# Optimization experiments

Measured on AMD Instinct MI355X. Metric: run time of the kernel, lower is better.

Reference implementation:

```python
import jax, jax.numpy as jnp
import numpy as np

BN_EPS = 1e-5
LRELU_SLOPE = 0.2


def setup_inputs() -> dict:
    key = jax.random.key(0)
    ks = jax.random.split(key, 8)
    B, N, D = 32, 2048, 64      # batch, nodes per graph, latent_dim
    E = 1_000_000               # num edges
    H = 128                     # edge_hidden_dim
    Din = 2 * D + 4             # concat(z_src, z_dst, edge_attr)
    z = jax.random.normal(ks[0], (B, N, D), dtype=jnp.float32)
    edge_index = jax.random.randint(ks[1], (2, E), 0, B * N, dtype=jnp.int64)
    edge_attr = jax.random.normal(ks[2], (E, 4), dtype=jnp.float32)
    W1 = jax.random.normal(ks[3], (Din, H), dtype=jnp.float32) * (1.0 / np.sqrt(Din))
    b1 = jnp.zeros((H,), dtype=jnp.float32)
    gamma = jnp.ones((H,), dtype=jnp.float32)
    beta = jnp.zeros((H,), dtype=jnp.float32)
    W2 = jax.random.normal(ks[4], (H, 1), dtype=jnp.float32) * (1.0 / np.sqrt(H))
    b2 = jnp.zeros((1,), dtype=jnp.float32)
    return {"z": z, "edge_attr": edge_attr, "W1": W1, "b1": b1,
            "gamma": gamma, "beta": beta, "W2": W2, "b2": b2,
            "edge_index": edge_index}


def reference(z, edge_attr, W1, b1, gamma, beta, W2, b2, edge_index):
    B, N, D = z.shape
    zf = z.reshape(-1, D)                       # [B*N, D]
    src, dst = edge_index[0], edge_index[1]
    edge_batch = jnp.clip(src // N, 0, B - 1)
    edge_offsets = edge_batch * N               # batch_offsets[edge_batch]
    src_idx = src % N + edge_offsets
    dst_idx = dst % N + edge_offsets
    edge_input = jnp.concatenate([zf[src_idx], zf[dst_idx], edge_attr], axis=1)  # [E, 2D+4]
    h = edge_input @ W1 + b1                    # [E, H]
    # BatchNorm1d (training mode: biased batch stats over edge dim)
    mu = jnp.mean(h, axis=0)
    var = jnp.mean(jnp.square(h - mu), axis=0)
    h = (h - mu) * jax.lax.rsqrt(var + BN_EPS) * gamma + beta
    h = jnp.where(h >= 0, h, LRELU_SLOPE * h)   # LeakyReLU(0.2)
    return h @ W2 + b2                          # [E, 1]
```

## Files before the change

### kernel.cpp

```cpp
#include <hip/hip_runtime.h>

#define E_EDGES   1000000
#define NNODES    2048
#define HCH       128
#define KP        136
#define TILE      64
#define NTILES    (E_EDGES / TILE)
#define NSPREAD   8
#define GRID_GEMM 1024
#define ZVEC      (32 * 2048 * 64 / 4)
#define ZBLK      2048
#define WBLK      66

typedef short  shortx8 __attribute__((ext_vector_type(8)));
typedef float  floatx4 __attribute__((ext_vector_type(4)));

__device__ __forceinline__ unsigned short f2bf(float f) {
  union { float f; unsigned int u; } v; v.f = f;
  unsigned int r = (v.u + 0x7fffu + ((v.u >> 16) & 1u)) >> 16;
  return (unsigned short)r;
}
__device__ __forceinline__ void cfence() { asm volatile("" ::: "memory"); }
__device__ __forceinline__ void bar_lds() {
  asm volatile("s_waitcnt lgkmcnt(0)" ::: "memory");
  __builtin_amdgcn_s_barrier();
  cfence();
}

__global__ void k_prep(const float* __restrict__ z, const float* __restrict__ W1,
                       const float* __restrict__ b1,
                       unsigned short* __restrict__ zb, unsigned short* __restrict__ w1t,
                       float* __restrict__ gstats) {
  int bid = blockIdx.x;
  if (bid < ZBLK) {
    const float4* z4 = (const float4*)z;
    ushort4* zb4 = (ushort4*)zb;
    for (int i = bid * 256 + threadIdx.x; i < ZVEC; i += ZBLK * 256) {
      float4 v = z4[i];
      ushort4 o;
      o.x = f2bf(v.x); o.y = f2bf(v.y); o.z = f2bf(v.z); o.w = f2bf(v.w);
      zb4[i] = o;
    }
  } else if (bid < ZBLK + WBLK) {
    int idx = (bid - ZBLK) * 256 + threadIdx.x;
    int k = idx >> 7, n = idx & 127;
    w1t[n * KP + k] = f2bf(W1[idx]);
  } else {
    int tid = threadIdx.x;
    if (tid < 512) {
      int n = tid >> 2, kp = 132 + (tid & 3);
      w1t[n * KP + kp] = (kp == 132) ? f2bf(b1[n]) : (unsigned short)0;
    }
    for (int i = tid; i < NSPREAD * 2 * HCH; i += 256) gstats[i] = 0.f;
  }
}

template<bool OUT>
__global__ __launch_bounds__(256, 4)
void k_gemm(const unsigned short* __restrict__ zb,
            const unsigned short* __restrict__ w1t,
            const int* __restrict__ ei,
            const float* __restrict__ attr,
            float* __restrict__ gstats,
            const float* __restrict__ gamma,
            const float* __restrict__ beta,
            const float* __restrict__ W2,
            const float* __restrict__ b2,
            float* __restrict__ out) {
  __shared__ __align__(16) unsigned short A[2][TILE * KP];
  __shared__ float po[2][4][TILE];

  const int tid  = threadIdx.x;
  const int lane = tid & 63;
  const int w    = tid >> 6;
  const int l15  = lane & 15;
  const int quad = lane >> 4;
  const int ea   = w * 8 + (lane >> 3);
  const int eb   = ea + 32;
  const int ch   = lane & 7;

  shortx8 bfr[2][4], bfr4[2];
#pragma unroll
  for (int nt = 0; nt < 2; ++nt) {
    const unsigned short* bp = w1t + (w * 32 + nt * 16 + l15) * KP;
#pragma unroll
    for (int kk = 0; kk < 4; ++kk)
      bfr[nt][kk] = *(const shortx8*)(bp + kk * 32 + quad * 8);
    bfr4[nt] = (quad == 0) ? *(const shortx8*)(bp + 128)
                           : (shortx8){0, 0, 0, 0, 0, 0, 0, 0};
  }

  float eaf[2], ebb[2], ew2[2], b2v = 0.f;
  float ssum[2] = {0.f, 0.f}, ssq[2] = {0.f, 0.f};
  if (OUT) {
#pragma unroll
    for (int nt = 0; nt < 2; ++nt) {
      int c = w * 32 + nt * 16 + l15;
      float S = 0.f, Q = 0.f;
#pragma unroll
      for (int i = 0; i < NSPREAD; ++i) {
        S += gstats[i * 2 * HCH + c];
        Q += gstats[i * 2 * HCH + HCH + c];
      }
      float mu   = S * (1.0f / (float)E_EDGES);
      float var  = Q * (1.0f / (float)E_EDGES) - mu * mu;
      float rstd = rsqrtf(var + 1e-5f);
      float a = gamma[c] * rstd;
      eaf[nt] = a;
      ebb[nt] = beta[c] - mu * a;
      ew2[nt] = W2[c];
    }
    b2v = b2[0];
  }

  if (tid < 128) {
    int b = tid >> 6, r = tid & 63;
    ushort4 bl; bl.x = 0x3F80; bl.y = 0; bl.z = 0; bl.w = 0;
    *(ushort4*)(&A[b][0] + r * KP + 132) = bl;
  }

  auto rows_of = [&](int s_a, int d_a, int s_b, int d_b,
                     unsigned& r0, unsigned& r1, unsigned& r2, unsigned& r3) {
    r0 = (unsigned)s_a;
    r1 = (unsigned)s_b;
    r2 = ((unsigned)s_a & ~(unsigned)(NNODES - 1)) | ((unsigned)d_a & (NNODES - 1));
    r3 = ((unsigned)s_b & ~(unsigned)(NNODES - 1)) | ((unsigned)d_b & (NNODES - 1));
  };

  const int t0 = blockIdx.x;
  uint4 g0, g1, g2, g3;
  float4 av;
  int sa, da, sb, db;
  {
    int s0a = ei[t0 * TILE + ea], d0a = ei[E_EDGES + t0 * TILE + ea];
    int s0b = ei[t0 * TILE + eb], d0b = ei[E_EDGES + t0 * TILE + eb];
    if (w == 0) av = ((const float4*)attr)[t0 * TILE + tid];
    unsigned r0, r1, r2, r3;
    rows_of(s0a, d0a, s0b, d0b, r0, r1, r2, r3);
    g0 = *(const uint4*)(zb + (size_t)r0 * 64 + ch * 8);
    g1 = *(const uint4*)(zb + (size_t)r1 * 64 + ch * 8);
    g2 = *(const uint4*)(zb + (size_t)r2 * 64 + ch * 8);
    g3 = *(const uint4*)(zb + (size_t)r3 * 64 + ch * 8);
    *(uint4*)(&A[0][0] + ea * KP + ch * 8)      = g0;
    *(uint4*)(&A[0][0] + eb * KP + ch * 8)      = g1;
    *(uint4*)(&A[0][0] + ea * KP + 64 + ch * 8) = g2;
    *(uint4*)(&A[0][0] + eb * KP + 64 + ch * 8) = g3;
    if (w == 0) {
      ushort4 a0; a0.x = f2bf(av.x); a0.y = f2bf(av.y);
      a0.z = f2bf(av.z); a0.w = f2bf(av.w);
      *(ushort4*)(&A[0][0] + tid * KP + 128) = a0;
    }
    int t1 = t0 + GRID_GEMM;
    int s1a = ei[t1 * TILE + ea], d1a = ei[E_EDGES + t1 * TILE + ea];
    int s1b = ei[t1 * TILE + eb], d1b = ei[E_EDGES + t1 * TILE + eb];
    rows_of(s1a, d1a, s1b, d1b, r0, r1, r2, r3);
    g0 = *(const uint4*)(zb + (size_t)r0 * 64 + ch * 8);
    g1 = *(const uint4*)(zb + (size_t)r1 * 64 + ch * 8);
    g2 = *(const uint4*)(zb + (size_t)r2 * 64 + ch * 8);
    g3 = *(const uint4*)(zb + (size_t)r3 * 64 + ch * 8);
    if (w == 0) av = ((const float4*)attr)[t1 * TILE + tid];
    int t2 = t0 + 2 * GRID_GEMM;
    sa = ei[t2 * TILE + ea]; da = ei[E_EDGES + t2 * TILE + ea];
    sb = ei[t2 * TILE + eb]; db = ei[E_EDGES + t2 * TILE + eb];
  }
  bar_lds();

  int pp = 0, sl = 0;
  for (int tile = t0; ; ) {
    const bool more = (tile + GRID_GEMM) < NTILES;

    if (more) {
      *(uint4*)(&A[pp ^ 1][0] + ea * KP + ch * 8)      = g0;
      *(uint4*)(&A[pp ^ 1][0] + eb * KP + ch * 8)      = g1;
      *(uint4*)(&A[pp ^ 1][0] + ea * KP + 64 + ch * 8) = g2;
      *(uint4*)(&A[pp ^ 1][0] + eb * KP + 64 + ch * 8) = g3;
      if (w == 0) {
        ushort4 a0; a0.x = f2bf(av.x); a0.y = f2bf(av.y);
        a0.z = f2bf(av.z); a0.w = f2bf(av.w);
        *(ushort4*)(&A[pp ^ 1][0] + tid * KP + 128) = a0;
      }
      unsigned r0, r1, r2, r3;
      rows_of(sa, da, sb, db, r0, r1, r2, r3);
      g0 = *(const uint4*)(zb + (size_t)r0 * 64 + ch * 8);
      g1 = *(const uint4*)(zb + (size_t)r1 * 64 + ch * 8);
      g2 = *(const uint4*)(zb + (size_t)r2 * 64 + ch * 8);
      g3 = *(const uint4*)(zb + (size_t)r3 * 64 + ch * 8);
      int tn2 = tile + 2 * GRID_GEMM; if (tn2 > NTILES - 1) tn2 = NTILES - 1;
      if (w == 0) av = ((const float4*)attr)[tn2 * TILE + tid];
      int tn3 = tile + 3 * GRID_GEMM; if (tn3 > NTILES - 1) tn3 = NTILES - 1;
      sa = ei[tn3 * TILE + ea]; da = ei[E_EDGES + tn3 * TILE + ea];
      sb = ei[tn3 * TILE + eb]; db = ei[E_EDGES + tn3 * TILE + eb];
    }

    const unsigned short* Ar = &A[pp][0];
#pragma unroll
    for (int mt = 0; mt < 4; ++mt) {
      const unsigned short* ap = Ar + (mt * 16 + l15) * KP;
      shortx8 afr[4], a4;
#pragma unroll
      for (int kk = 0; kk < 4; ++kk)
        afr[kk] = *(const shortx8*)(ap + kk * 32 + quad * 8);
      a4 = (quad == 0) ? *(const shortx8*)(ap + 128)
                       : (shortx8){0, 0, 0, 0, 0, 0, 0, 0};

      floatx4 acc[2];
      acc[0] = (floatx4){0.f, 0.f, 0.f, 0.f};
      acc[1] = (floatx4){0.f, 0.f, 0.f, 0.f};
#pragma unroll
      for (int kk = 0; kk < 4; ++kk)
#pragma unroll
        for (int nt = 0; nt < 2; ++nt)
          acc[nt] = __builtin_amdgcn_mfma_f32_16x16x32_bf16(
              afr[kk], bfr[nt][kk], acc[nt], 0, 0, 0);
#pragma unroll
      for (int nt = 0; nt < 2; ++nt)
        acc[nt] = __builtin_amdgcn_mfma_f32_16x16x32_bf16(
            a4, bfr4[nt], acc[nt], 0, 0, 0);

      if (!OUT) {
#pragma unroll
        for (int nt = 0; nt < 2; ++nt) {
          float s = 0.f, qq = 0.f;
#pragma unroll
          for (int r = 0; r < 4; ++r) {
            float h = acc[nt][r];
            s += h; qq += h * h;
          }
          ssum[nt] += s; ssq[nt] += qq;
        }
      } else {
#pragma unroll
        for (int r = 0; r < 4; ++r) {
          float t = 0.f;
#pragma unroll
          for (int nt = 0; nt < 2; ++nt) {
            float h = acc[nt][r];
            float p = fmaf(eaf[nt], h, ebb[nt]);
            p = (p >= 0.f) ? p : 0.2f * p;
            t = fmaf(ew2[nt], p, t);
          }
          t += __shfl_xor(t, 1);
          t += __shfl_xor(t, 2);
          t += __shfl_xor(t, 4);
          t += __shfl_xor(t, 8);
          if (l15 == 0)
            po[sl][w][mt * 16 + quad * 4 + r] = t;
        }
      }
    }

    if (more || OUT) bar_lds();

    if (OUT && tid < TILE)
      out[tile * TILE + tid] = po[sl][0][tid] + po[sl][1][tid] +
                               po[sl][2][tid] + po[sl][3][tid] + b2v;

    if (!more) break;
    pp ^= 1; sl ^= 1;
    tile += GRID_GEMM;
  }

  if (!OUT) {
    float* gs = gstats + (blockIdx.x & (NSPREAD - 1)) * 2 * HCH;
#pragma unroll
    for (int nt = 0; nt < 2; ++nt) {
      float s = ssum[nt], qq = ssq[nt];
      s += __shfl_xor(s, 16); s += __shfl_xor(s, 32);
      qq += __shfl_xor(qq, 16); qq += __shfl_xor(qq, 32);
      if (quad == 0) {
        int c = w * 32 + nt * 16 + l15;
        atomicAdd(&gs[c], s);
        atomicAdd(&gs[HCH + c], qq);
      }
    }
  }
}

extern "C" void kernel_launch(void* const* d_in, const int* in_sizes, int n_in,
                              void* d_out, int out_size, void* d_ws, size_t ws_size,
                              hipStream_t stream) {
  const float* z     = (const float*)d_in[0];
  const float* attr  = (const float*)d_in[1];
  const float* W1    = (const float*)d_in[2];
  const float* b1    = (const float*)d_in[3];
  const float* gamma = (const float*)d_in[4];
  const float* beta  = (const float*)d_in[5];
  const float* W2    = (const float*)d_in[6];
  const float* b2    = (const float*)d_in[7];
  const int*   ei    = (const int*)d_in[8];
  float* out = (float*)d_out;

  char* ws = (char*)d_ws;
  unsigned short* zb  = (unsigned short*)ws;
  unsigned short* w1t = (unsigned short*)(ws + 8388608);
  float* gstats       = (float*)(ws + 8423424);

  k_prep<<<ZBLK + WBLK + 1, 256, 0, stream>>>(z, W1, b1, zb, w1t, gstats);
  k_gemm<false><<<GRID_GEMM, 256, 0, stream>>>(zb, w1t, ei, attr, gstats,
                                               gamma, beta, W2, b2, nullptr);
  k_gemm<true><<<GRID_GEMM, 256, 0, stream>>>(zb, w1t, ei, attr, gstats,
                                              gamma, beta, W2, b2, out);
}
```

Measured before the change: 210.5 us.

## Bin edges by source graph group so each XCD gathers from an L2-resident z slice

Adds a count/scan/scatter pre-pass that sorts edges into 8 bins by source-node range. It packs each edge into a 16-byte record: both row indices, the bf16 edge attributes and the original edge id. The GEMM blocks are mapped to bins via blockIdx&7, so each group of co-scheduled blocks gathers from roughly a 1 MB slice of the bf16 z table. The aim is to turn random gathers into mostly L2 hits. The cost is three extra small kernels, an extra read and write of all edges, and scattered output writes through the stashed edge ids.

```diff
diff --git a/kernel.cpp b/kernel.cpp
--- a/kernel.cpp
+++ b/kernel.cpp
@@ -8,9 +8,12 @@
 #define NTILES    (E_EDGES / TILE)
 #define NSPREAD   8
 #define GRID_GEMM 1024
+#define BPB       128
 #define ZVEC      (32 * 2048 * 64 / 4)
 #define ZBLK      2048
 #define WBLK      66
+#define NBIN      8
+#define CBLK      512
 
 typedef short  shortx8 __attribute__((ext_vector_type(8)));
 typedef float  floatx4 __attribute__((ext_vector_type(4)));
@@ -26,11 +29,16 @@
   __builtin_amdgcn_s_barrier();
   cfence();
 }
+__device__ __forceinline__ unsigned pack_rows(int s, int d) {
+  unsigned rs = (unsigned)s & 0xFFFFu;
+  unsigned rd = (unsigned)(((s & ~(NNODES - 1)) | (d & (NNODES - 1)))) & 0xFFFFu;
+  return rs | (rd << 16);
+}
 
 __global__ void k_prep(const float* __restrict__ z, const float* __restrict__ W1,
-                       const float* __restrict__ b1,
+                       const float* __restrict__ b1, const int* __restrict__ ei,
                        unsigned short* __restrict__ zb, unsigned short* __restrict__ w1t,
-                       float* __restrict__ gstats) {
+                       float* __restrict__ gstats, int* __restrict__ cnt) {
   int bid = blockIdx.x;
   if (bid < ZBLK) {
     const float4* z4 = (const float4*)z;
@@ -45,13 +53,71 @@
     int idx = (bid - ZBLK) * 256 + threadIdx.x;
     int k = idx >> 7, n = idx & 127;
     w1t[n * KP + k] = f2bf(W1[idx]);
-  } else {
+  } else if (bid == ZBLK + WBLK) {
     int tid = threadIdx.x;
     if (tid < 512) {
       int n = tid >> 2, kp = 132 + (tid & 3);
       w1t[n * KP + kp] = (kp == 132) ? f2bf(b1[n]) : (unsigned short)0;
     }
     for (int i = tid; i < NSPREAD * 2 * HCH; i += 256) gstats[i] = 0.f;
+  } else {
+    __shared__ int lh[NBIN];
+    int tid = threadIdx.x;
+    int cb = bid - (ZBLK + WBLK + 1);
+    if (tid < NBIN) lh[tid] = 0;
+    __syncthreads();
+    for (int e = cb * 256 + tid; e < E_EDGES; e += CBLK * 256)
+      atomicAdd(&lh[((unsigned)ei[e]) >> 13], 1);
+    __syncthreads();
+    if (tid < NBIN) cnt[cb * NBIN + tid] = lh[tid];
+  }
+}
+
+__global__ void k_scan(const int* __restrict__ cnt, int* __restrict__ base,
+                       int* __restrict__ binTile) {
+  __shared__ int tot[NBIN], S[NBIN + 1];
+  int b = threadIdx.x;
+  if (b < NBIN) {
+    int t = 0;
+    for (int blk = 0; blk < CBLK; ++blk) t += cnt[blk * NBIN + b];
+    tot[b] = t;
+  }
+  __syncthreads();
+  if (b == 0) {
+    int a = 0;
+    for (int i = 0; i < NBIN; ++i) { S[i] = a; a += tot[i]; }
+    S[NBIN] = a;
+    binTile[0] = 0;
+    for (int i = 1; i <= NBIN; ++i) binTile[i] = (S[i] + 63) >> 6;
+  }
+  __syncthreads();
+  if (b < NBIN) {
+    int run = S[b];
+    for (int blk = 0; blk < CBLK; ++blk) {
+      base[blk * NBIN + b] = run;
+      run += cnt[blk * NBIN + b];
+    }
+  }
+}
+
+__global__ __launch_bounds__(256)
+void k_scatter(const int* __restrict__ ei, const float* __restrict__ attr,
+               const int* __restrict__ base, uint4* __restrict__ recs) {
+  __shared__ int lcnt[NBIN];
+  int tid = threadIdx.x, bid = blockIdx.x;
+  if (tid < NBIN) lcnt[tid] = base[bid * NBIN + tid];
+  __syncthreads();
+  for (int e = bid * 256 + tid; e < E_EDGES; e += CBLK * 256) {
+    int s = ei[e], d = ei[E_EDGES + e];
+    float4 a = ((const float4*)attr)[e];
+    int b = ((unsigned)s) >> 13;
+    int slot = atomicAdd(&lcnt[b], 1);
+    uint4 r;
+    r.x = pack_rows(s, d);
+    r.y = (unsigned)f2bf(a.x) | ((unsigned)f2bf(a.y) << 16);
+    r.z = (unsigned)f2bf(a.z) | ((unsigned)f2bf(a.w) << 16);
+    r.w = (unsigned)e;
+    recs[slot] = r;
   }
 }
 
@@ -59,8 +125,8 @@
 __global__ __launch_bounds__(256, 4)
 void k_gemm(const unsigned short* __restrict__ zb,
             const unsigned short* __restrict__ w1t,
-            const int* __restrict__ ei,
-            const float* __restrict__ attr,
+            const uint4* __restrict__ recs,
+            const int* __restrict__ binTile,
             float* __restrict__ gstats,
             const float* __restrict__ gamma,
             const float* __restrict__ beta,
@@ -69,6 +135,7 @@
             float* __restrict__ out) {
   __shared__ __align__(16) unsigned short A[2][TILE * KP];
   __shared__ float po[2][4][TILE];
+  __shared__ int ostash[3][TILE];
 
   const int tid  = threadIdx.x;
   const int lane = tid & 63;
@@ -119,77 +186,75 @@
     *(ushort4*)(&A[b][0] + r * KP + 132) = bl;
   }
 
-  auto rows_of = [&](int s_a, int d_a, int s_b, int d_b,
-                     unsigned& r0, unsigned& r1, unsigned& r2, unsigned& r3) {
-    r0 = (unsigned)s_a;
-    r1 = (unsigned)s_b;
-    r2 = ((unsigned)s_a & ~(unsigned)(NNODES - 1)) | ((unsigned)d_a & (NNODES - 1));
-    r3 = ((unsigned)s_b & ~(unsigned)(NNODES - 1)) | ((unsigned)d_b & (NNODES - 1));
+  const int x    = blockIdx.x & 7;
+  const int t0i  = binTile[x] + (blockIdx.x >> 3);
+  const int tEnd = binTile[x + 1];
+  if (t0i >= tEnd) return;
+
+  auto stage = [&](uint4 ra, uint4 rb, const uint4& h0, const uint4& h1,
+                   const uint4& h2, const uint4& h3, int buf, int os) {
+    *(uint4*)(&A[buf][0] + ea * KP + ch * 8)      = h0;
+    *(uint4*)(&A[buf][0] + eb * KP + ch * 8)      = h1;
+    *(uint4*)(&A[buf][0] + ea * KP + 64 + ch * 8) = h2;
+    *(uint4*)(&A[buf][0] + eb * KP + 64 + ch * 8) = h3;
+    if (ch == 0) {
+      ushort4 aA; aA.x = (unsigned short)ra.y; aA.y = (unsigned short)(ra.y >> 16);
+      aA.z = (unsigned short)ra.z; aA.w = (unsigned short)(ra.z >> 16);
+      *(ushort4*)(&A[buf][0] + ea * KP + 128) = aA;
+      ushort4 aB; aB.x = (unsigned short)rb.y; aB.y = (unsigned short)(rb.y >> 16);
+      aB.z = (unsigned short)rb.z; aB.w = (unsigned short)(rb.z >> 16);
+      *(ushort4*)(&A[buf][0] + eb * KP + 128) = aB;
+      ostash[os][ea] = (int)ra.w;
+      ostash[os][eb] = (int)rb.w;
+    }
   };
 
-  const int t0 = blockIdx.x;
   uint4 g0, g1, g2, g3;
-  float4 av;
-  int sa, da, sb, db;
+  uint4 recSa, recSb;
+  uint4 recFa, recFb;
   {
-    int s0a = ei[t0 * TILE + ea], d0a = ei[E_EDGES + t0 * TILE + ea];
-    int s0b = ei[t0 * TILE + eb], d0b = ei[E_EDGES + t0 * TILE + eb];
-    if (w == 0) av = ((const float4*)attr)[t0 * TILE + tid];
-    unsigned r0, r1, r2, r3;
-    rows_of(s0a, d0a, s0b, d0b, r0, r1, r2, r3);
+    uint4 ra = recs[t0i * TILE + ea];
+    uint4 rb = recs[t0i * TILE + eb];
+    unsigned r0 = ra.x & 0xFFFFu, r1 = rb.x & 0xFFFFu;
+    unsigned r2 = ra.x >> 16,     r3 = rb.x >> 16;
+    uint4 h0 = *(const uint4*)(zb + (size_t)r0 * 64 + ch * 8);
+    uint4 h1 = *(const uint4*)(zb + (size_t)r1 * 64 + ch * 8);
+    uint4 h2 = *(const uint4*)(zb + (size_t)r2 * 64 + ch * 8);
+    uint4 h3 = *(const uint4*)(zb + (size_t)r3 * 64 + ch * 8);
+    stage(ra, rb, h0, h1, h2, h3, 0, 0);
+    int t1 = t0i + BPB; if (t1 > tEnd - 1) t1 = tEnd - 1;
+    recSa = recs[t1 * TILE + ea];
+    recSb = recs[t1 * TILE + eb];
+    r0 = recSa.x & 0xFFFFu; r1 = recSb.x & 0xFFFFu;
+    r2 = recSa.x >> 16;     r3 = recSb.x >> 16;
     g0 = *(const uint4*)(zb + (size_t)r0 * 64 + ch * 8);
     g1 = *(const uint4*)(zb + (size_t)r1 * 64 + ch * 8);
     g2 = *(const uint4*)(zb + (size_t)r2 * 64 + ch * 8);
     g3 = *(const uint4*)(zb + (size_t)r3 * 64 + ch * 8);
-    *(uint4*)(&A[0][0] + ea * KP + ch * 8)      = g0;
-    *(uint4*)(&A[0][0] + eb * KP + ch * 8)      = g1;
-    *(uint4*)(&A[0][0] + ea * KP + 64 + ch * 8) = g2;
-    *(uint4*)(&A[0][0] + eb * KP + 64 + ch * 8) = g3;
-    if (w == 0) {
-      ushort4 a0; a0.x = f2bf(av.x); a0.y = f2bf(av.y);
-      a0.z = f2bf(av.z); a0.w = f2bf(av.w);
-      *(ushort4*)(&A[0][0] + tid * KP + 128) = a0;
-    }
-    int t1 = t0 + GRID_GEMM;
-    int s1a = ei[t1 * TILE + ea], d1a = ei[E_EDGES + t1 * TILE + ea];
-    int s1b = ei[t1 * TILE + eb], d1b = ei[E_EDGES + t1 * TILE + eb];
-    rows_of(s1a, d1a, s1b, d1b, r0, r1, r2, r3);
-    g0 = *(const uint4*)(zb + (size_t)r0 * 64 + ch * 8);
-    g1 = *(const uint4*)(zb + (size_t)r1 * 64 + ch * 8);
-    g2 = *(const uint4*)(zb + (size_t)r2 * 64 + ch * 8);
-    g3 = *(const uint4*)(zb + (size_t)r3 * 64 + ch * 8);
-    if (w == 0) av = ((const float4*)attr)[t1 * TILE + tid];
-    int t2 = t0 + 2 * GRID_GEMM;
-    sa = ei[t2 * TILE + ea]; da = ei[E_EDGES + t2 * TILE + ea];
-    sb = ei[t2 * TILE + eb]; db = ei[E_EDGES + t2 * TILE + eb];
+    int t2 = t0i + 2 * BPB; if (t2 > tEnd - 1) t2 = tEnd - 1;
+    recFa = recs[t2 * TILE + ea];
+    recFb = recs[t2 * TILE + eb];
   }
   bar_lds();
 
-  int pp = 0, sl = 0;
-  for (int tile = t0; ; ) {
-    const bool more = (tile + GRID_GEMM) < NTILES;
+  int pp = 0, sl = 0, osr = 0;
+  for (int tile = t0i; ; ) {
+    const int tnext = tile + BPB;
+    const bool more = tnext < tEnd;
+    const int osw = (osr == 2) ? 0 : osr + 1;
 
     if (more) {
-      *(uint4*)(&A[pp ^ 1][0] + ea * KP + ch * 8)      = g0;
-      *(uint4*)(&A[pp ^ 1][0] + eb * KP + ch * 8)      = g1;
-      *(uint4*)(&A[pp ^ 1][0] + ea * KP + 64 + ch * 8) = g2;
-      *(uint4*)(&A[pp ^ 1][0] + eb * KP + 64 + ch * 8) = g3;
-      if (w == 0) {
-        ushort4 a0; a0.x = f2bf(av.x); a0.y = f2bf(av.y);
-        a0.z = f2bf(av.z); a0.w = f2bf(av.w);
-        *(ushort4*)(&A[pp ^ 1][0] + tid * KP + 128) = a0;
-      }
-      unsigned r0, r1, r2, r3;
-      rows_of(sa, da, sb, db, r0, r1, r2, r3);
+      stage(recSa, recSb, g0, g1, g2, g3, pp ^ 1, osw);
+      unsigned r0 = recFa.x & 0xFFFFu, r1 = recFb.x & 0xFFFFu;
+      unsigned r2 = recFa.x >> 16,     r3 = recFb.x >> 16;
       g0 = *(const uint4*)(zb + (size_t)r0 * 64 + ch * 8);
       g1 = *(const uint4*)(zb + (size_t)r1 * 64 + ch * 8);
       g2 = *(const uint4*)(zb + (size_t)r2 * 64 + ch * 8);
       g3 = *(const uint4*)(zb + (size_t)r3 * 64 + ch * 8);
-      int tn2 = tile + 2 * GRID_GEMM; if (tn2 > NTILES - 1) tn2 = NTILES - 1;
-      if (w == 0) av = ((const float4*)attr)[tn2 * TILE + tid];
-      int tn3 = tile + 3 * GRID_GEMM; if (tn3 > NTILES - 1) tn3 = NTILES - 1;
-      sa = ei[tn3 * TILE + ea]; da = ei[E_EDGES + tn3 * TILE + ea];
-      sb = ei[tn3 * TILE + eb]; db = ei[E_EDGES + tn3 * TILE + eb];
+      recSa = recFa; recSb = recFb;
+      int tn3 = tile + 3 * BPB; if (tn3 > tEnd - 1) tn3 = tEnd - 1;
+      recFa = recs[tn3 * TILE + ea];
+      recFb = recs[tn3 * TILE + eb];
     }
 
     const unsigned short* Ar = &A[pp][0];
@@ -252,12 +317,12 @@
     if (more || OUT) bar_lds();
 
     if (OUT && tid < TILE)
-      out[tile * TILE + tid] = po[sl][0][tid] + po[sl][1][tid] +
-                               po[sl][2][tid] + po[sl][3][tid] + b2v;
+      out[ostash[osr][tid]] = po[sl][0][tid] + po[sl][1][tid] +
+                              po[sl][2][tid] + po[sl][3][tid] + b2v;
 
     if (!more) break;
-    pp ^= 1; sl ^= 1;
-    tile += GRID_GEMM;
+    pp ^= 1; sl ^= 1; osr = osw;
+    tile = tnext;
   }
 
   if (!OUT) {
@@ -294,10 +359,17 @@
   unsigned short* zb  = (unsigned short*)ws;
   unsigned short* w1t = (unsigned short*)(ws + 8388608);
   float* gstats       = (float*)(ws + 8423424);
-
-  k_prep<<<ZBLK + WBLK + 1, 256, 0, stream>>>(z, W1, b1, zb, w1t, gstats);
-  k_gemm<false><<<GRID_GEMM, 256, 0, stream>>>(zb, w1t, ei, attr, gstats,
+  int* cnt            = (int*)(ws + 8431616);
+  int* base           = (int*)(ws + 8448000);
+  int* binTile        = (int*)(ws + 8464384);
+  uint4* recs         = (uint4*)(ws + 8464448);
+
+  k_prep<<<ZBLK + WBLK + 1 + CBLK, 256, 0, stream>>>(z, W1, b1, ei, zb, w1t,
+                                                     gstats, cnt);
+  k_scan<<<1, 64, 0, stream>>>(cnt, base, binTile);
+  k_scatter<<<CBLK, 256, 0, stream>>>(ei, attr, base, recs);
+  k_gemm<false><<<GRID_GEMM, 256, 0, stream>>>(zb, w1t, recs, binTile, gstats,
                                                gamma, beta, W2, b2, nullptr);
-  k_gemm<true><<<GRID_GEMM, 256, 0, stream>>>(zb, w1t, ei, attr, gstats,
+  k_gemm<true><<<GRID_GEMM, 256, 0, stream>>>(zb, w1t, recs, binTile, gstats,
                                               gamma, beta, W2, b2, out);
 }
```

After: 261.5 us. 1.24x slower.
